# Performance work log

Measured on AMD Instinct MI355X. Metric: run time of the kernel, lower is better.

## Reference

```python
import jax, jax.numpy as jnp
import numpy as np

SEQ, D, H = 4096, 1024, 1024


def setup_inputs() -> dict:
    key = jax.random.key(0)
    k_x, k_w1, k_b1, k_w2, k_b2 = jax.random.split(key, 5)
    std = 1.0 / np.sqrt(H)
    inputs = jax.random.normal(k_x, (SEQ, D), dtype=jnp.float32)
    W1 = jax.random.uniform(k_w1, (3 * H, 2 * D), minval=-std, maxval=std, dtype=jnp.float32)
    b1 = jax.random.uniform(k_b1, (3 * H,), minval=-std, maxval=std, dtype=jnp.float32)
    W2 = jax.random.uniform(k_w2, (H, H), minval=-std, maxval=std, dtype=jnp.float32)
    b2 = jax.random.uniform(k_b2, (H,), minval=-std, maxval=std, dtype=jnp.float32)
    return {"inputs": inputs, "W1": W1, "b1": b1, "W2": W2, "b2": b2}


def reference(inputs, W1, b1, W2, b2):
    # Exclusive prefix sum along seq: s[t] = sum_{i<t} x[i]
    s = jnp.concatenate(
        [jnp.zeros((1, inputs.shape[1]), dtype=inputs.dtype),
         jnp.cumsum(inputs[:-1], axis=0)], axis=0)
    v = jnp.concatenate([inputs, s], axis=1)            # [S, 2D]
    gates = v @ W1.T + b1                               # [S, 3H]
    ig, fg, h = jnp.split(gates, 3, axis=1)
    ig = jax.nn.sigmoid(ig)
    fg = jax.nn.sigmoid(fg)
    h = jnp.tanh(h) @ W2.T + b2                         # [S, H]
    hr = h * ig
    return (fg, hr)
```

## Files before the change

kernel.cpp:

```cpp
#include <hip/hip_runtime.h>
#include <cmath>

#define S_SEQ 4096
#define HD 1024
#define NG 3072
#define CHR 32
#define NCH 128

typedef _Float16 half8_t __attribute__((ext_vector_type(8)));
typedef _Float16 half4_t __attribute__((ext_vector_type(4)));
typedef float f32x4_t __attribute__((ext_vector_type(4)));

__device__ __forceinline__ void gload_lds16(const void* g, void* l) {
  __builtin_amdgcn_global_load_lds(
      (const __attribute__((address_space(1))) void*)g,
      (__attribute__((address_space(3))) void*)l, 16, 0, 0);
}

__device__ __forceinline__ float sigmoidf_(float x) {
  return 1.f / (1.f + __expf(-x));
}
__device__ __forceinline__ float tanhf_(float x) {
  return 1.f - 2.f / (__expf(2.f * x) + 1.f);
}

__global__ void conv_f32_f16(const float* __restrict__ src,
                             _Float16* __restrict__ dst, int n4) {
  int i = blockIdx.x * 256 + threadIdx.x;
  if (i >= n4) return;
  float4 v = *(const float4*)(src + (size_t)i * 4);
  half4_t h;
  h[0] = (_Float16)v.x; h[1] = (_Float16)v.y;
  h[2] = (_Float16)v.z; h[3] = (_Float16)v.w;
  *(half4_t*)(dst + (size_t)i * 4) = h;
}

__global__ void scan_x(const float* __restrict__ x, _Float16* __restrict__ A,
                       _Float16* __restrict__ xsum) {
  int j = blockIdx.x * 256 + threadIdx.x;
  int c = blockIdx.y;
  int t0 = c * CHR;
  float run = 0.f;
  for (int t = t0; t < t0 + CHR; ++t) {
    float v = x[(size_t)t * HD + j];
    A[(size_t)t * 2048 + j]        = (_Float16)v;
    A[(size_t)t * 2048 + 1024 + j] = (_Float16)run;
    run += v;
  }
  xsum[(size_t)c * HD + j] = (_Float16)run;
}

__global__ void scan_part(const float* __restrict__ praw,
                          const float* __restrict__ b1,
                          float* __restrict__ pout) {
  int j = blockIdx.x * 256 + threadIdx.x;
  float run = b1[j];
  for (int c = 0; c < NCH; ++c) {
    float v = praw[(size_t)c * NG + j];
    pout[(size_t)c * NG + j] = run;
    run += v;
  }
}

template <int MODE>
__global__ __launch_bounds__(256, 2)
void gemm_bt(const _Float16* __restrict__ A, const _Float16* __restrict__ B,
             int M, int N, int K, int ldb,
             float* __restrict__ C,
             const float* __restrict__ bias, const _Float16* __restrict__ mulh,
             float* __restrict__ out,
             const float* __restrict__ part, _Float16* __restrict__ igb,
             _Float16* __restrict__ th) {
  __shared__ _Float16 As[128 * 32];
  __shared__ _Float16 Bs[128 * 32];

  const int tid = threadIdx.x;
  const int lane = tid & 63;
  const int wid = tid >> 6;
  const int wr = wid >> 1;
  const int wc = wid & 1;

  const int m0 = blockIdx.y * 128;
  const int n0 = blockIdx.x * 128;

  const int srow = lane >> 2;
  const int scol = (lane & 3) << 3;

  const _Float16* gA = A + (size_t)(m0 + wid * 32 + srow) * K + scol;
  const _Float16* gB = B + (size_t)(n0 + wid * 32 + srow) * ldb + scol;
  _Float16* lA = As + (wid * 32) * 32;
  _Float16* lB = Bs + (wid * 32) * 32;

  f32x4_t acc[4][4] = {};

  const int fr = lane & 15;
  const int fk = (lane >> 4) << 3;

  for (int kk = 0; kk < K; kk += 32) {
    gload_lds16(gA + kk,                  lA);
    gload_lds16(gA + kk + (size_t)16*K,   lA + 16 * 32);
    gload_lds16(gB + kk,                  lB);
    gload_lds16(gB + kk + (size_t)16*ldb, lB + 16 * 32);
    __syncthreads();

    half8_t af[4], bf[4];
#pragma unroll
    for (int m = 0; m < 4; ++m)
      af[m] = *(const half8_t*)&As[(wr * 64 + m * 16 + fr) * 32 + fk];
#pragma unroll
    for (int n = 0; n < 4; ++n)
      bf[n] = *(const half8_t*)&Bs[(wc * 64 + n * 16 + fr) * 32 + fk];
#pragma unroll
    for (int m = 0; m < 4; ++m)
#pragma unroll
      for (int n = 0; n < 4; ++n)
        acc[m][n] = __builtin_amdgcn_mfma_f32_16x16x32_f16(af[m], bf[n],
                                                           acc[m][n], 0, 0, 0);
    __syncthreads();
  }

  const int crow = m0 + wr * 64 + ((lane >> 4) << 2);
  const int ccol = n0 + wc * 64 + (lane & 15);
#pragma unroll
  for (int m = 0; m < 4; ++m)
#pragma unroll
    for (int n = 0; n < 4; ++n) {
      const int col = ccol + n * 16;
#pragma unroll
      for (int r = 0; r < 4; ++r) {
        const int row = crow + m * 16 + r;
        const float v = acc[m][n][r];
        if (MODE == 0) {
          C[(size_t)row * N + col] = v;
        } else if (MODE == 1) {
          size_t idx = (size_t)row * N + col;
          out[idx] = (v + bias[col]) * (float)mulh[idx];
        } else {
          float g = v + part[(size_t)(row >> 5) * NG + col];
          if (col < 1024)
            igb[(size_t)row * HD + col] = (_Float16)sigmoidf_(g);
          else if (col < 2048)
            out[(size_t)row * HD + (col - 1024)] = sigmoidf_(g);
          else
            th[(size_t)row * HD + (col - 2048)] = (_Float16)tanhf_(g);
        }
      }
    }
}

extern "C" void kernel_launch(void* const* d_in, const int* in_sizes, int n_in,
                              void* d_out, int out_size, void* d_ws, size_t ws_size,
                              hipStream_t stream) {
  const float* x  = (const float*)d_in[0];
  const float* W1 = (const float*)d_in[1];
  const float* b1 = (const float*)d_in[2];
  const float* W2 = (const float*)d_in[3];
  const float* b2 = (const float*)d_in[4];
  float* out0 = (float*)d_out;
  float* out1 = out0 + (size_t)S_SEQ * HD;

  char* ws = (char*)d_ws;
  _Float16* Ah    = (_Float16*)(ws);
  _Float16* w1h   = (_Float16*)(ws + ((size_t)16 << 20));
  _Float16* w2h   = (_Float16*)(ws + ((size_t)28 << 20));
  _Float16* xsumh = (_Float16*)(ws + ((size_t)30 << 20));
  float*    praw  = (float*)   (ws + ((size_t)31 << 20));
  float*    pout  = (float*)   (ws + ((size_t)33 << 20));
  _Float16* igb   = (_Float16*)(ws + ((size_t)35 << 20));
  _Float16* th    = (_Float16*)(ws + ((size_t)43 << 20));

  conv_f32_f16<<<dim3(6144), dim3(256), 0, stream>>>(W1, w1h, NG * 2048 / 4);
  conv_f32_f16<<<dim3(1024), dim3(256), 0, stream>>>(W2, w2h, HD * HD / 4);

  scan_x<<<dim3(4, NCH), dim3(256), 0, stream>>>(x, Ah, xsumh);

  gemm_bt<0><<<dim3(NG / 128, 1), dim3(256), 0, stream>>>(
      xsumh, w1h + 1024, NCH, NG, HD, 2048,
      praw, nullptr, nullptr, nullptr, nullptr, nullptr, nullptr);

  scan_part<<<dim3(NG / 256), dim3(256), 0, stream>>>(praw, b1, pout);

  gemm_bt<2><<<dim3(NG / 128, S_SEQ / 128), dim3(256), 0, stream>>>(
      Ah, w1h, S_SEQ, NG, 2048, 2048,
      nullptr, nullptr, nullptr, out0, pout, igb, th);

  gemm_bt<1><<<dim3(HD / 128, S_SEQ / 128), dim3(256), 0, stream>>>(
      th, w2h, S_SEQ, HD, HD, HD,
      nullptr, b2, igb, out1, nullptr, nullptr, nullptr);
}
```

Before: 153.9 us.

## Replace main gate GEMM with 256x256 double-buffered 8-phase pipelined kernel

The large gate GEMM (4096x3072x2048) moves from a simple 128x128 tile kernel with a full sync every 32-wide K step to a dedicated 512-thread kernel. The new kernel uses 256x256 tiles, a 64-wide K step and double-buffered LDS filled by direct global-to-LDS loads. Compute is split into eight phases that interleave LDS fragment reads, next-stage prefetch and MFMA bursts, with barriers, setprio and partial vmcnt waits. It also XOR-swizzles LDS to avoid bank conflicts and remaps block IDs for L2 locality. The aim is to hide memory latency and raise MFMA utilisation, at the cost of 128KB LDS per block, more register pressure and only 192 blocks in the grid.

```diff
diff --git a/kernel.cpp b/kernel.cpp
--- a/kernel.cpp
+++ b/kernel.cpp
@@ -6,6 +6,8 @@
 #define NG 3072
 #define CHR 32
 #define NCH 128
+#define K1 2048
+#define NT1 (K1 / 64)
 
 typedef _Float16 half8_t __attribute__((ext_vector_type(8)));
 typedef _Float16 half4_t __attribute__((ext_vector_type(4)));
@@ -68,9 +70,7 @@
              int M, int N, int K, int ldb,
              float* __restrict__ C,
              const float* __restrict__ bias, const _Float16* __restrict__ mulh,
-             float* __restrict__ out,
-             const float* __restrict__ part, _Float16* __restrict__ igb,
-             _Float16* __restrict__ th) {
+             float* __restrict__ out) {
   __shared__ _Float16 As[128 * 32];
   __shared__ _Float16 Bs[128 * 32];
 
@@ -132,20 +132,155 @@
         const float v = acc[m][n][r];
         if (MODE == 0) {
           C[(size_t)row * N + col] = v;
-        } else if (MODE == 1) {
+        } else {
           size_t idx = (size_t)row * N + col;
           out[idx] = (v + bias[col]) * (float)mulh[idx];
-        } else {
-          float g = v + part[(size_t)(row >> 5) * NG + col];
-          if (col < 1024)
-            igb[(size_t)row * HD + col] = (_Float16)sigmoidf_(g);
-          else if (col < 2048)
-            out[(size_t)row * HD + (col - 1024)] = sigmoidf_(g);
-          else
-            th[(size_t)row * HD + (col - 2048)] = (_Float16)tanhf_(g);
         }
       }
     }
+}
+
+#define BARX __builtin_amdgcn_s_barrier()
+#define PR1 __builtin_amdgcn_s_setprio(1)
+#define PR0 __builtin_amdgcn_s_setprio(0)
+#define VM8 asm volatile("s_waitcnt vmcnt(8)" ::: "memory")
+
+__global__ __launch_bounds__(512, 2)
+void gemm1_8ph(const _Float16* __restrict__ A, const _Float16* __restrict__ B,
+               const float* __restrict__ part, _Float16* __restrict__ igb,
+               float* __restrict__ out0, _Float16* __restrict__ th) {
+  __shared__ __align__(16) _Float16 sA[2][256 * 64];
+  __shared__ __align__(16) _Float16 sB[2][256 * 64];
+
+  const int tid = threadIdx.x;
+  const int l = tid & 63;
+  const int w = tid >> 6;
+  const int wr = w >> 2;
+  const int wc = w & 3;
+
+  const int id = blockIdx.x;
+  const int swz = (id & 7) * 24 + (id >> 3);
+  const int bx = swz % 12;
+  const int by = swz / 12;
+  const int m0 = by * 256;
+  const int n0 = bx * 256;
+
+  const int lr = l >> 3;
+  const int lcs = ((l & 7) ^ lr) << 3;
+  const _Float16* gAb = A + (size_t)(m0 + w * 32 + lr) * K1 + lcs;
+  const _Float16* gBb = B + (size_t)(n0 + w * 32 + lr) * K1 + lcs;
+  const int ldso = (w * 32) * 64;
+
+#define STAGE(buf, kk) do {                                                   \
+    _Pragma("unroll")                                                         \
+    for (int j = 0; j < 4; ++j)                                               \
+      gload_lds16(gAb + (kk) + j * 8 * K1, (_Float16*)&sA[buf][ldso + j*512]);\
+    _Pragma("unroll")                                                         \
+    for (int j = 0; j < 4; ++j)                                               \
+      gload_lds16(gBb + (kk) + j * 8 * K1, (_Float16*)&sB[buf][ldso + j*512]);\
+  } while (0)
+
+#define LDA(AF, MH, buf) do {                                                 \
+    _Pragma("unroll")                                                         \
+    for (int m = 0; m < 4; ++m) {                                             \
+      int row = wr * 128 + (MH) * 64 + m * 16 + (l & 15);                     \
+      int k0 = (l >> 4) << 3;                                                 \
+      int sw = (row & 7) << 3;                                                \
+      AF[m][0] = *(const half8_t*)&sA[buf][(row * 64 + k0) ^ sw];             \
+      AF[m][1] = *(const half8_t*)&sA[buf][(row * 64 + 32 + k0) ^ sw];        \
+    }                                                                         \
+  } while (0)
+
+#define LDB_(BF, NH, buf) do {                                                \
+    _Pragma("unroll")                                                         \
+    for (int n = 0; n < 2; ++n) {                                             \
+      int row = wc * 64 + (NH) * 32 + n * 16 + (l & 15);                      \
+      int k0 = (l >> 4) << 3;                                                 \
+      int sw = (row & 7) << 3;                                                \
+      BF[n][0] = *(const half8_t*)&sB[buf][(row * 64 + k0) ^ sw];             \
+      BF[n][1] = *(const half8_t*)&sB[buf][(row * 64 + 32 + k0) ^ sw];        \
+    }                                                                         \
+  } while (0)
+
+#define MM(MH, NH, AF, BF) do {                                               \
+    _Pragma("unroll")                                                         \
+    for (int m = 0; m < 4; ++m)                                               \
+      _Pragma("unroll")                                                       \
+      for (int n = 0; n < 2; ++n) {                                           \
+        acc[MH][NH][m][n] = __builtin_amdgcn_mfma_f32_16x16x32_f16(           \
+            AF[m][0], BF[n][0], acc[MH][NH][m][n], 0, 0, 0);                  \
+        acc[MH][NH][m][n] = __builtin_amdgcn_mfma_f32_16x16x32_f16(           \
+            AF[m][1], BF[n][1], acc[MH][NH][m][n], 0, 0, 0);                  \
+      }                                                                       \
+  } while (0)
+
+  f32x4_t acc[2][2][4][2] = {};
+
+  STAGE(0, 0);
+  STAGE(1, 64);
+  VM8; BARX;
+
+  for (int it = 0; it < NT1 / 2; ++it) {
+    const int kn0 = it * 128 + 128;
+    const int kn1 = it * 128 + 192;
+    const int s0 = (kn0 < K1) ? kn0 : (K1 - 64);
+    const int s1 = (kn1 < K1) ? kn1 : (K1 - 64);
+
+    half8_t a0[4][2], a1[4][2], b0[2][2], b1[2][2];
+
+    LDA(a0, 0, 0); LDB_(b0, 0, 0);
+    BARX; PR1; MM(0, 0, a0, b0); PR0; BARX;
+
+    LDB_(b1, 1, 0);
+    BARX; PR1; MM(0, 1, a0, b1); PR0; BARX;
+
+    LDA(a1, 1, 0);
+    BARX; PR1; MM(1, 0, a1, b0); PR0; BARX;
+
+    STAGE(0, s0);
+    BARX; PR1; MM(1, 1, a1, b1); PR0; VM8; BARX;
+
+    LDA(a0, 0, 1); LDB_(b0, 0, 1);
+    BARX; PR1; MM(0, 0, a0, b0); PR0; BARX;
+
+    LDB_(b1, 1, 1);
+    BARX; PR1; MM(0, 1, a0, b1); PR0; BARX;
+
+    LDA(a1, 1, 1);
+    BARX; PR1; MM(1, 0, a1, b0); PR0; BARX;
+
+    STAGE(1, s1);
+    BARX; PR1; MM(1, 1, a1, b1); PR0; VM8; BARX;
+  }
+
+  const int region = n0 >> 10;
+  const int cb = n0 & 1023;
+#pragma unroll
+  for (int mh = 0; mh < 2; ++mh)
+#pragma unroll
+    for (int m = 0; m < 4; ++m) {
+      const int rbase = m0 + wr * 128 + mh * 64 + m * 16 + ((l >> 4) << 2);
+#pragma unroll
+      for (int r = 0; r < 4; ++r) {
+        const int grow = rbase + r;
+        const float* prow = part + (size_t)(grow >> 5) * NG + n0;
+#pragma unroll
+        for (int nh = 0; nh < 2; ++nh)
+#pragma unroll
+          for (int n = 0; n < 2; ++n) {
+            const int lc = wc * 64 + nh * 32 + n * 16 + (l & 15);
+            const float g = acc[mh][nh][m][n][r] + prow[lc];
+            const size_t oi = (size_t)grow * HD + cb + lc;
+            if (region == 0)      igb[oi] = (_Float16)sigmoidf_(g);
+            else if (region == 1) out0[oi] = sigmoidf_(g);
+            else                  th[oi] = (_Float16)tanhf_(g);
+          }
+      }
+    }
+#undef STAGE
+#undef LDA
+#undef LDB_
+#undef MM
 }
 
 extern "C" void kernel_launch(void* const* d_in, const int* in_sizes, int n_in,
@@ -175,16 +310,12 @@
   scan_x<<<dim3(4, NCH), dim3(256), 0, stream>>>(x, Ah, xsumh);
 
   gemm_bt<0><<<dim3(NG / 128, 1), dim3(256), 0, stream>>>(
-      xsumh, w1h + 1024, NCH, NG, HD, 2048,
-      praw, nullptr, nullptr, nullptr, nullptr, nullptr, nullptr);
+      xsumh, w1h + 1024, NCH, NG, HD, 2048, praw, nullptr, nullptr, nullptr);
 
   scan_part<<<dim3(NG / 256), dim3(256), 0, stream>>>(praw, b1, pout);
 
-  gemm_bt<2><<<dim3(NG / 128, S_SEQ / 128), dim3(256), 0, stream>>>(
-      Ah, w1h, S_SEQ, NG, 2048, 2048,
-      nullptr, nullptr, nullptr, out0, pout, igb, th);
+  gemm1_8ph<<<dim3(192), dim3(512), 0, stream>>>(Ah, w1h, pout, igb, out0, th);
 
   gemm_bt<1><<<dim3(HD / 128, S_SEQ / 128), dim3(256), 0, stream>>>(
-      th, w2h, S_SEQ, HD, HD, HD,
-      nullptr, b2, igb, out1, nullptr, nullptr, nullptr);
-}
+      th, w2h, S_SEQ, HD, HD, HD, nullptr, b2, igb, out1);
+}
```

Result: slower. 157.9 us (+2.6%).
